# Kernel optimization log

Measured on AMD Instinct MI355X. Metric: run time of the kernel, lower is better.

Reference implementation:

```python
import jax, jax.numpy as jnp
import numpy as np

KERNEL_MUL = 2.0
KERNEL_NUM = 5


def setup_inputs() -> dict:
    key = jax.random.key(0)
    k1, k2 = jax.random.split(key)
    source = jax.random.normal(k1, (4096, 512), dtype=jnp.float32)
    target = jax.random.normal(k2, (4096, 512), dtype=jnp.float32)
    return {"source": source, "target": target}


def reference(source, target):
    B = source.shape[0]
    src = source.reshape(B, -1)
    tgt = target.reshape(B, -1)
    total = jnp.concatenate([src, tgt], axis=0)  # [2B, D]
    n = 2 * B

    # Pairwise squared L2 via ||a||^2 + ||b||^2 - 2 a.b (GEMM trick)
    sq = jnp.sum(total * total, axis=-1)  # [2B]
    d2 = sq[:, None] + sq[None, :] - 2.0 * (total @ total.T)  # [2B, 2B]
    d2 = jnp.maximum(d2, 0.0)

    # Median-heuristic-style bandwidth; torch uses L2_distance.data (no grad)
    bandwidth = jax.lax.stop_gradient(jnp.sum(d2)) / (n * n - n)
    bandwidth = bandwidth / (KERNEL_MUL ** (KERNEL_NUM // 2))

    # Multi-bandwidth Gaussian kernel sum
    kernels = jnp.zeros_like(d2)
    for i in range(KERNEL_NUM):
        kernels = kernels + jnp.exp(-d2 / (bandwidth * (KERNEL_MUL ** i)))

    XX = kernels[:B, :B]
    YY = kernels[B:, B:]
    XY = kernels[:B, B:]
    YX = kernels[B:, :B]
    return jnp.mean(XX + YY - XY - YX)
```

## Files before the change

### kernel.cpp

```cpp
#include <hip/hip_runtime.h>


typedef int i32x4 __attribute__((ext_vector_type(4)));

#define N_TOT  8192
#define DIM    512
#define BM     128
#define TILES  64
#define NPAIRS 2080
#define QSCALE 24.0f
#define FP_OFF 295040
#define IMG_OFF 327680ULL

__device__ __forceinline__ int q8(float x) {
    int q = __float2int_rn(x * QSCALE);
    return max(-127, min(127, q));
}

__global__ __launch_bounds__(256) void k_pre(
    const float* __restrict__ src, const float* __restrict__ tgt,
    unsigned char* __restrict__ img,
    float* __restrict__ sq, float* __restrict__ v)
{
    __shared__ __align__(16) signed char qt[BM][80];
    const int b = blockIdx.x;
    const int p = b >> 3, kp = b & 7;
    const int t = threadIdx.x;
    const float* base = ((p < 32) ? src + (size_t)p * BM * DIM
                                  : tgt + (size_t)(p - 32) * BM * DIM) + kp * 64;
    {
        int r = t >> 1, ch = (t & 1) * 32;
        const float* qp = base + (size_t)r * DIM + ch;
        float rsq = 0.f;
        #pragma unroll
        for (int j = 0; j < 8; ++j) {
            float4 x = *(const float4*)(qp + j * 4);
            int q0 = q8(x.x), q1 = q8(x.y), q2 = q8(x.z), q3 = q8(x.w);
            unsigned int w = (q0 & 255) | ((q1 & 255) << 8) | ((q2 & 255) << 16)
                             | ((unsigned)(q3 & 255) << 24);
            *(unsigned int*)&qt[r][ch + j * 4] = w;
            rsq += (float)(q0 * q0 + q1 * q1 + q2 * q2 + q3 * q3);
        }
        rsq += __shfl_xor(rsq, 1);
        if ((t & 1) == 0) atomicAdd(&sq[p * BM + r], rsq);
    }
    __syncthreads();
    #pragma unroll
    for (int h = 0; h < 2; ++h) {
        int ci = t + h * 256;
        int g = ci >> 6, lane = ci & 63;
        int row = g * 16 + (lane & 15), c0 = (lane >> 4) * 16;
        uint4 w = *(const uint4*)&qt[row][c0];
        *(uint4*)(img + (size_t)p * 65536 + (size_t)kp * 8192
                  + (size_t)g * 1024 + (size_t)lane * 16) = w;
    }
    if (t < 64) {
        float s = 0.f;
        for (int r = 0; r < BM; ++r) s += (float)qt[r][t];
        atomicAdd(&v[kp * 64 + t], s);
    }
}

__global__ __launch_bounds__(256, 4) void kmain(
    const unsigned char* __restrict__ img,
    const float* __restrict__ sq, const float* __restrict__ vv_,
    float* __restrict__ Fpart)
{
    __shared__ float red[4], redS[4], redV[4];

    int b = blockIdx.x;
    int s = (b & 7) * (NPAIRS / 8) + (b >> 3);
    int SI = 0, rem = s;
    while (rem >= 10 + 16 * (15 - SI)) { rem -= 10 + 16 * (15 - SI); ++SI; }
    int I, J;
    if (rem < 10) {
        int di = 0;
        while (rem >= 4 - di) { rem -= 4 - di; ++di; }
        I = SI * 4 + di; J = SI * 4 + di + rem;
    } else {
        rem -= 10;
        int SJ = SI + 1 + (rem >> 4);
        I = SI * 4 + ((rem >> 2) & 3);
        J = SJ * 4 + (rem & 3);
    }

    const int tid  = threadIdx.x;
    const int lane = tid & 63;
    const int wid  = tid >> 6;
    const int wr   = wid >> 1, wc = wid & 1;
    const int lhi  = lane >> 4, llo = lane & 15;

    const char* gA = (const char*)img + (size_t)I * 65536;
    const char* gB = (const char*)img + (size_t)J * 65536;
    const int vA = wr * 4096 + lane * 16;
    const int vB = wc * 4096 + lane * 16;

    float Sp = 0.f;
    #pragma unroll
    for (int i = 0; i < 32; ++i) Sp += sq[tid + i * 256];
    float Vp;
    { float v0 = vv_[tid], v1 = vv_[tid + 256]; Vp = v0 * v0 + v1 * v1; }
    #pragma unroll
    for (int off = 32; off > 0; off >>= 1) {
        Sp += __shfl_down(Sp, off);
        Vp += __shfl_down(Vp, off);
    }
    if (lane == 0) { redS[wid] = Sp; redV[wid] = Vp; }
    __syncthreads();
    float S = redS[0] + redS[1] + redS[2] + redS[3];
    float V = redV[0] + redV[1] + redV[2] + redV[3];
    float sumd2 = 2.f * (float)N_TOT * S - 2.f * V;
    float bw = sumd2 / ((float)N_TOT * (float)N_TOT - (float)N_TOT) * 0.25f;
    const float c = 1.4426950408889634f / (16.f * bw);

    i32x4 acc[4][4];
    #pragma unroll
    for (int m = 0; m < 4; ++m)
        #pragma unroll
        for (int n = 0; n < 4; ++n) acc[m][n] = (i32x4){0, 0, 0, 0};

    #pragma unroll
    for (int kp = 0; kp < 8; ++kp) {
        i32x4 aF[4], bF[4];
        #pragma unroll
        for (int m = 0; m < 4; ++m) {
            aF[m] = *(const i32x4*)(gA + (size_t)kp * 8192 + m * 1024 + vA);
            bF[m] = *(const i32x4*)(gB + (size_t)kp * 8192 + m * 1024 + vB);
        }
        #pragma unroll
        for (int m = 0; m < 4; ++m)
            #pragma unroll
            for (int n = 0; n < 4; ++n)
                acc[m][n] = __builtin_amdgcn_mfma_i32_16x16x64_i8(
                    aF[m], bF[n], acc[m][n], 0, 0, 0);
    }

    const int rI = I * BM, rJ = J * BM;
    float sqc_[4];
    #pragma unroll
    for (int n = 0; n < 4; ++n)
        sqc_[n] = sq[rJ + wc * 64 + n * 16 + llo];

    float local = 0.f;
    #pragma unroll
    for (int m = 0; m < 4; ++m) {
        float sqr_[4];
        #pragma unroll
        for (int r = 0; r < 4; ++r)
            sqr_[r] = sq[rI + wr * 64 + m * 16 + lhi * 4 + r];
        #pragma unroll
        for (int n = 0; n < 4; ++n)
            #pragma unroll
            for (int r = 0; r < 4; ++r) {
                float d2 = fmaf(-2.f, (float)acc[m][n][r], sqr_[r] + sqc_[n]);
                float u = __builtin_amdgcn_exp2f(-d2 * c);
                float u2 = u * u, u4 = u2 * u2, u8 = u4 * u4, u16 = u8 * u8;
                local += u + u2 + u4 + u8 + u16;
            }
    }

    float wgt = ((I < 32) == (J < 32)) ? 1.f : -1.f;
    if (I != J) wgt *= 2.f;
    local *= wgt;

    #pragma unroll
    for (int off = 32; off > 0; off >>= 1) local += __shfl_down(local, off);
    if (lane == 0) red[wid] = local;
    __syncthreads();
    if (tid == 0) Fpart[b] = red[0] + red[1] + red[2] + red[3];
}

__global__ void k4_out(const float* __restrict__ Fpart, float* __restrict__ out) {
    int t = threadIdx.x;
    double s = 0.0;
    for (int i = t; i < NPAIRS; i += 256) s += (double)Fpart[i];
    #pragma unroll
    for (int off = 32; off > 0; off >>= 1) s += __shfl_down(s, off);
    __shared__ double r[4];
    if ((t & 63) == 0) r[t >> 6] = s;
    __syncthreads();
    if (t == 0) out[0] = (float)((r[0] + r[1] + r[2] + r[3]) / ((double)4096 * 4096.0));
}

extern "C" void kernel_launch(void* const* d_in, const int* in_sizes, int n_in,
                              void* d_out, int out_size, void* d_ws, size_t ws_size,
                              hipStream_t stream) {
    const float* src = (const float*)d_in[0];
    const float* tgt = (const float*)d_in[1];
    char* ws = (char*)d_ws;
    float* sq    = (float*)ws;
    float* v     = (float*)(ws + 32768);
    float* Fpart = (float*)(ws + FP_OFF);
    unsigned char* img = (unsigned char*)(ws + IMG_OFF);
    float* out = (float*)d_out;

    hipMemsetAsync(ws, 0, 34816, stream);
    hipLaunchKernelGGL(k_pre, dim3(512), dim3(256), 0, stream, src, tgt, img, sq, v);
    hipLaunchKernelGGL(kmain, dim3(NPAIRS), dim3(256), 0, stream, img, sq, v, Fpart);
    hipLaunchKernelGGL(k4_out, dim3(1), dim3(256), 0, stream, Fpart, out);
}
```

Baseline: 51.65 us.

## Process two column tiles per block to reuse A fragments

Each block now computes two 128x128 output tiles (I,J1) and (I,J1+1) sharing the same A-row fragments, halving the grid to 1056 blocks. The diagonal tile is handled by masking the lower triangle inside the tile and weighting the upper triangle by two. This is meant to cut A-fragment global loads and per-block setup such as the bandwidth reduction. In exchange it doubles the accumulator registers, drops launch bounds to 2 waves per SIMD, and leaves a padded dummy tile for the last row.

```diff
diff --git a/kernel.cpp b/kernel.cpp
--- a/kernel.cpp
+++ b/kernel.cpp
@@ -6,8 +6,7 @@
 #define N_TOT  8192
 #define DIM    512
 #define BM     128
-#define TILES  64
-#define NPAIRS 2080
+#define NPB    1056
 #define QSCALE 24.0f
 #define FP_OFF 295040
 #define IMG_OFF 327680ULL
@@ -61,7 +60,42 @@
     }
 }
 
-__global__ __launch_bounds__(256, 4) void kmain(
+#define EPILOG(ACC, JJ, WGT)                                                   \
+    do {                                                                       \
+        const int rJ_ = (JJ) * BM;                                             \
+        float sqc_[4];                                                         \
+        _Pragma("unroll")                                                      \
+        for (int n = 0; n < 4; ++n)                                            \
+            sqc_[n] = sq[rJ_ + wc * 64 + n * 16 + llo];                        \
+        float psum = 0.f;                                                      \
+        _Pragma("unroll")                                                      \
+        for (int m = 0; m < 4; ++m) {                                          \
+            float sqr_[4];                                                     \
+            _Pragma("unroll")                                                  \
+            for (int r = 0; r < 4; ++r)                                        \
+                sqr_[r] = sq[rI + wr * 64 + m * 16 + lhi * 4 + r];             \
+            _Pragma("unroll")                                                  \
+            for (int n = 0; n < 4; ++n)                                        \
+                _Pragma("unroll")                                              \
+                for (int r = 0; r < 4; ++r) {                                  \
+                    float d2 = fmaf(-2.f, (float)ACC[m][n][r],                 \
+                                    sqr_[r] + sqc_[n]);                        \
+                    float u = __builtin_amdgcn_exp2f(-d2 * c);                 \
+                    float u2 = u * u, u4 = u2 * u2, u8 = u4 * u4,              \
+                          u16 = u8 * u8;                                       \
+                    float k5 = u + u2 + u4 + u8 + u16;                         \
+                    if (diag1 && (&ACC[0][0] == &acc1[0][0])) {                \
+                        int ri = wr * 64 + m * 16 + lhi * 4 + r;               \
+                        int cj = wc * 64 + n * 16 + llo;                       \
+                        k5 *= (cj > ri) ? 2.f : ((cj == ri) ? 1.f : 0.f);      \
+                    }                                                          \
+                    psum += k5;                                                \
+                }                                                              \
+        }                                                                      \
+        local += (WGT) * psum;                                                 \
+    } while (0)
+
+__global__ __launch_bounds__(256, 2) void kmain(
     const unsigned char* __restrict__ img,
     const float* __restrict__ sq, const float* __restrict__ vv_,
     float* __restrict__ Fpart)
@@ -69,20 +103,13 @@
     __shared__ float red[4], redS[4], redV[4];
 
     int b = blockIdx.x;
-    int s = (b & 7) * (NPAIRS / 8) + (b >> 3);
-    int SI = 0, rem = s;
-    while (rem >= 10 + 16 * (15 - SI)) { rem -= 10 + 16 * (15 - SI); ++SI; }
-    int I, J;
-    if (rem < 10) {
-        int di = 0;
-        while (rem >= 4 - di) { rem -= 4 - di; ++di; }
-        I = SI * 4 + di; J = SI * 4 + di + rem;
-    } else {
-        rem -= 10;
-        int SJ = SI + 1 + (rem >> 4);
-        I = SI * 4 + ((rem >> 2) & 3);
-        J = SJ * 4 + (rem & 3);
-    }
+    int s = (b & 7) * (NPB / 8) + (b >> 3);
+    int I = 0;
+    while (s >= ((65 - I) >> 1)) { s -= (65 - I) >> 1; ++I; }
+    const int J1 = I + 2 * s;
+    const int J2 = J1 + 1;
+    const bool has2 = (J2 < 64);
+    const int J2a = has2 ? J2 : J1;
 
     const int tid  = threadIdx.x;
     const int lane = tid & 63;
@@ -90,8 +117,9 @@
     const int wr   = wid >> 1, wc = wid & 1;
     const int lhi  = lane >> 4, llo = lane & 15;
 
-    const char* gA = (const char*)img + (size_t)I * 65536;
-    const char* gB = (const char*)img + (size_t)J * 65536;
+    const char* gA  = (const char*)img + (size_t)I   * 65536;
+    const char* gB1 = (const char*)img + (size_t)J1  * 65536;
+    const char* gB2 = (const char*)img + (size_t)J2a * 65536;
     const int vA = wr * 4096 + lane * 16;
     const int vB = wc * 4096 + lane * 16;
 
@@ -113,55 +141,46 @@
     float bw = sumd2 / ((float)N_TOT * (float)N_TOT - (float)N_TOT) * 0.25f;
     const float c = 1.4426950408889634f / (16.f * bw);
 
-    i32x4 acc[4][4];
+    i32x4 acc1[4][4], acc2[4][4];
     #pragma unroll
     for (int m = 0; m < 4; ++m)
         #pragma unroll
-        for (int n = 0; n < 4; ++n) acc[m][n] = (i32x4){0, 0, 0, 0};
+        for (int n = 0; n < 4; ++n) {
+            acc1[m][n] = (i32x4){0, 0, 0, 0};
+            acc2[m][n] = (i32x4){0, 0, 0, 0};
+        }
 
     #pragma unroll
     for (int kp = 0; kp < 8; ++kp) {
-        i32x4 aF[4], bF[4];
+        i32x4 aF[4], b1F[4], b2F[4];
         #pragma unroll
         for (int m = 0; m < 4; ++m) {
-            aF[m] = *(const i32x4*)(gA + (size_t)kp * 8192 + m * 1024 + vA);
-            bF[m] = *(const i32x4*)(gB + (size_t)kp * 8192 + m * 1024 + vB);
+            aF[m]  = *(const i32x4*)(gA  + (size_t)kp * 8192 + m * 1024 + vA);
+            b1F[m] = *(const i32x4*)(gB1 + (size_t)kp * 8192 + m * 1024 + vB);
+            b2F[m] = *(const i32x4*)(gB2 + (size_t)kp * 8192 + m * 1024 + vB);
         }
         #pragma unroll
         for (int m = 0; m < 4; ++m)
             #pragma unroll
-            for (int n = 0; n < 4; ++n)
-                acc[m][n] = __builtin_amdgcn_mfma_i32_16x16x64_i8(
-                    aF[m], bF[n], acc[m][n], 0, 0, 0);
-    }
-
-    const int rI = I * BM, rJ = J * BM;
-    float sqc_[4];
-    #pragma unroll
-    for (int n = 0; n < 4; ++n)
-        sqc_[n] = sq[rJ + wc * 64 + n * 16 + llo];
-
+            for (int n = 0; n < 4; ++n) {
+                acc1[m][n] = __builtin_amdgcn_mfma_i32_16x16x64_i8(
+                    aF[m], b1F[n], acc1[m][n], 0, 0, 0);
+                acc2[m][n] = __builtin_amdgcn_mfma_i32_16x16x64_i8(
+                    aF[m], b2F[n], acc2[m][n], 0, 0, 0);
+            }
+    }
+
+    const int rI = I * BM;
+    const bool diag1 = (J1 == I);
     float local = 0.f;
-    #pragma unroll
-    for (int m = 0; m < 4; ++m) {
-        float sqr_[4];
-        #pragma unroll
-        for (int r = 0; r < 4; ++r)
-            sqr_[r] = sq[rI + wr * 64 + m * 16 + lhi * 4 + r];
-        #pragma unroll
-        for (int n = 0; n < 4; ++n)
-            #pragma unroll
-            for (int r = 0; r < 4; ++r) {
-                float d2 = fmaf(-2.f, (float)acc[m][n][r], sqr_[r] + sqc_[n]);
-                float u = __builtin_amdgcn_exp2f(-d2 * c);
-                float u2 = u * u, u4 = u2 * u2, u8 = u4 * u4, u16 = u8 * u8;
-                local += u + u2 + u4 + u8 + u16;
-            }
-    }
-
-    float wgt = ((I < 32) == (J < 32)) ? 1.f : -1.f;
-    if (I != J) wgt *= 2.f;
-    local *= wgt;
+
+    float w1 = ((I < 32) == (J1 < 32)) ? 1.f : -1.f;
+    if (!diag1) w1 *= 2.f;
+    EPILOG(acc1, J1, w1);
+
+    float w2 = ((I < 32) == (J2a < 32)) ? 2.f : -2.f;
+    if (!has2) w2 = 0.f;
+    EPILOG(acc2, J2a, w2);
 
     #pragma unroll
     for (int off = 32; off > 0; off >>= 1) local += __shfl_down(local, off);
@@ -173,7 +192,7 @@
 __global__ void k4_out(const float* __restrict__ Fpart, float* __restrict__ out) {
     int t = threadIdx.x;
     double s = 0.0;
-    for (int i = t; i < NPAIRS; i += 256) s += (double)Fpart[i];
+    for (int i = t; i < NPB; i += 256) s += (double)Fpart[i];
     #pragma unroll
     for (int off = 32; off > 0; off >>= 1) s += __shfl_down(s, off);
     __shared__ double r[4];
@@ -196,6 +215,6 @@
 
     hipMemsetAsync(ws, 0, 34816, stream);
     hipLaunchKernelGGL(k_pre, dim3(512), dim3(256), 0, stream, src, tgt, img, sq, v);
-    hipLaunchKernelGGL(kmain, dim3(NPAIRS), dim3(256), 0, stream, img, sq, v, Fpart);
+    hipLaunchKernelGGL(kmain, dim3(NPB), dim3(256), 0, stream, img, sq, v, Fpart);
     hipLaunchKernelGGL(k4_out, dim3(1), dim3(256), 0, stream, Fpart, out);
 }
```

New measurement: 55.73 us. +7.9%, slower.

## Switch int8 GEMM tiles to 32x32x32 MFMA with matching image layout

Applied to the files above, without the earlier changes.

Repacks the quantized int8 image into 32-row by 32-byte fragments and replaces the 16x16x64 MFMA tiling with 32x32x32 MFMAs, halving per-step global fragment loads per wave. The epilogue is remapped to the 32x32 accumulator layout. Diagonal tiles now apply an upper-triangle weighting per element, which adds branch and arithmetic work on those tiles.

```diff
diff --git a/kernel.cpp b/kernel.cpp
--- a/kernel.cpp
+++ b/kernel.cpp
@@ -1,12 +1,12 @@
 #include <hip/hip_runtime.h>
 
 
-typedef int i32x4 __attribute__((ext_vector_type(4)));
+typedef int i32x4  __attribute__((ext_vector_type(4)));
+typedef int i32x16 __attribute__((ext_vector_type(16)));
 
 #define N_TOT  8192
 #define DIM    512
 #define BM     128
-#define TILES  64
 #define NPAIRS 2080
 #define QSCALE 24.0f
 #define FP_OFF 295040
@@ -48,11 +48,12 @@
     #pragma unroll
     for (int h = 0; h < 2; ++h) {
         int ci = t + h * 256;
-        int g = ci >> 6, lane = ci & 63;
-        int row = g * 16 + (lane & 15), c0 = (lane >> 4) * 16;
-        uint4 w = *(const uint4*)&qt[row][c0];
-        *(uint4*)(img + (size_t)p * 65536 + (size_t)kp * 8192
-                  + (size_t)g * 1024 + (size_t)lane * 16) = w;
+        int kc = ci >> 8, rg = (ci >> 6) & 3, lane = ci & 63;
+        int row = rg * 32 + (lane & 31);
+        int col = kc * 32 + (lane >> 5) * 16;
+        uint4 w = *(const uint4*)&qt[row][col];
+        *(uint4*)(img + (size_t)p * 65536 + (size_t)(kp * 2 + kc) * 4096
+                  + (size_t)rg * 1024 + (size_t)lane * 16) = w;
     }
     if (t < 64) {
         float s = 0.f;
@@ -88,12 +89,12 @@
     const int lane = tid & 63;
     const int wid  = tid >> 6;
     const int wr   = wid >> 1, wc = wid & 1;
-    const int lhi  = lane >> 4, llo = lane & 15;
+    const int l31  = lane & 31, hi32 = lane >> 5;
 
     const char* gA = (const char*)img + (size_t)I * 65536;
     const char* gB = (const char*)img + (size_t)J * 65536;
-    const int vA = wr * 4096 + lane * 16;
-    const int vB = wc * 4096 + lane * 16;
+    const int vA = wr * 2048 + lane * 16;
+    const int vB = wc * 2048 + lane * 16;
 
     float Sp = 0.f;
     #pragma unroll
@@ -113,49 +114,57 @@
     float bw = sumd2 / ((float)N_TOT * (float)N_TOT - (float)N_TOT) * 0.25f;
     const float c = 1.4426950408889634f / (16.f * bw);
 
-    i32x4 acc[4][4];
-    #pragma unroll
-    for (int m = 0; m < 4; ++m)
-        #pragma unroll
-        for (int n = 0; n < 4; ++n) acc[m][n] = (i32x4){0, 0, 0, 0};
-
-    #pragma unroll
-    for (int kp = 0; kp < 8; ++kp) {
-        i32x4 aF[4], bF[4];
-        #pragma unroll
-        for (int m = 0; m < 4; ++m) {
-            aF[m] = *(const i32x4*)(gA + (size_t)kp * 8192 + m * 1024 + vA);
-            bF[m] = *(const i32x4*)(gB + (size_t)kp * 8192 + m * 1024 + vB);
+    i32x16 acc[2][2];
+    #pragma unroll
+    for (int m = 0; m < 2; ++m)
+        #pragma unroll
+        for (int n = 0; n < 2; ++n)
+            #pragma unroll
+            for (int r = 0; r < 16; ++r) acc[m][n][r] = 0;
+
+    #pragma unroll
+    for (int kc = 0; kc < 16; ++kc) {
+        i32x4 aF[2], bF[2];
+        #pragma unroll
+        for (int m = 0; m < 2; ++m) {
+            aF[m] = *(const i32x4*)(gA + (size_t)kc * 4096 + m * 1024 + vA);
+            bF[m] = *(const i32x4*)(gB + (size_t)kc * 4096 + m * 1024 + vB);
         }
         #pragma unroll
-        for (int m = 0; m < 4; ++m)
+        for (int m = 0; m < 2; ++m)
             #pragma unroll
-            for (int n = 0; n < 4; ++n)
-                acc[m][n] = __builtin_amdgcn_mfma_i32_16x16x64_i8(
+            for (int n = 0; n < 2; ++n)
+                acc[m][n] = __builtin_amdgcn_mfma_i32_32x32x32_i8(
                     aF[m], bF[n], acc[m][n], 0, 0, 0);
     }
 
     const int rI = I * BM, rJ = J * BM;
-    float sqc_[4];
-    #pragma unroll
-    for (int n = 0; n < 4; ++n)
-        sqc_[n] = sq[rJ + wc * 64 + n * 16 + llo];
+    float sqc_[2];
+    #pragma unroll
+    for (int n = 0; n < 2; ++n)
+        sqc_[n] = sq[rJ + wc * 64 + n * 32 + l31];
 
     float local = 0.f;
     #pragma unroll
-    for (int m = 0; m < 4; ++m) {
-        float sqr_[4];
-        #pragma unroll
-        for (int r = 0; r < 4; ++r)
-            sqr_[r] = sq[rI + wr * 64 + m * 16 + lhi * 4 + r];
-        #pragma unroll
-        for (int n = 0; n < 4; ++n)
+    for (int m = 0; m < 2; ++m) {
+        float sqr_[16];
+        #pragma unroll
+        for (int r = 0; r < 16; ++r)
+            sqr_[r] = sq[rI + wr * 64 + m * 32 + (r & 3) + 8 * (r >> 2) + 4 * hi32];
+        #pragma unroll
+        for (int n = 0; n < 2; ++n)
             #pragma unroll
-            for (int r = 0; r < 4; ++r) {
+            for (int r = 0; r < 16; ++r) {
                 float d2 = fmaf(-2.f, (float)acc[m][n][r], sqr_[r] + sqc_[n]);
                 float u = __builtin_amdgcn_exp2f(-d2 * c);
                 float u2 = u * u, u4 = u2 * u2, u8 = u4 * u4, u16 = u8 * u8;
-                local += u + u2 + u4 + u8 + u16;
+                float k5 = u + u2 + u4 + u8 + u16;
+                if (I == J) {
+                    int ri = wr * 64 + m * 32 + (r & 3) + 8 * (r >> 2) + 4 * hi32;
+                    int cj = wc * 64 + n * 32 + l31;
+                    k5 *= (cj > ri) ? 2.f : ((cj == ri) ? 1.f : 0.f);
+                }
+                local += k5;
             }
     }
 
```

Result: slower. 58.42 us (+13.1%).
